# Performance work log

Hardware: AMD Instinct MI355X
Metric: run time of the kernel (lower is better)

## Reference

```python
import jax, jax.numpy as jnp
import numpy as np

N_NODES = 50000
N_EDGES = 800000
IN_DIM, HID_DIM, OUT_DIM = 128, 96, 96
NUM_GRAPHS = 64
NEG_SLOPE_ATT = 0.2   # GATConv internal leaky_relu
NEG_SLOPE_ACT = 0.01  # F.leaky_relu default between layers


def setup_inputs() -> dict:
    key = jax.random.key(0)
    ks = jax.random.split(key, 16)
    x = jax.random.normal(ks[0], (N_NODES, IN_DIM), dtype=jnp.float32)
    edge_index = jax.random.randint(ks[1], (2, N_EDGES), 0, N_NODES, dtype=jnp.int64)
    batch = jnp.sort(jax.random.randint(ks[2], (N_NODES,), 0, NUM_GRAPHS, dtype=jnp.int64))

    def glorot(k, shape):
        lim = np.sqrt(6.0 / (shape[0] + shape[-1]))
        return jax.random.uniform(k, shape, jnp.float32, -lim, lim)

    params = {}
    dims = [(IN_DIM, HID_DIM), (HID_DIM, HID_DIM), (HID_DIM, OUT_DIM)]
    for i, (di, do) in enumerate(dims, start=1):
        params[f"W{i}"] = glorot(ks[3 * i], (di, do))
        params[f"a_src{i}"] = glorot(ks[3 * i + 1], (do,))
        params[f"a_dst{i}"] = glorot(ks[3 * i + 2], (do,))
        params[f"b{i}"] = jnp.zeros((do,), jnp.float32)
    return {"x": x, "edge_index": edge_index, "batch": batch, **params}


def gat_conv(x, src, dst, W, a_src, a_dst, b):
    # x: [N, in], src/dst: [Etot] (self-loops included)
    h = x @ W                                   # [N, out]
    alpha_s = h @ a_src                         # [N]
    alpha_d = h @ a_dst                         # [N]
    e = jax.nn.leaky_relu(alpha_s[src] + alpha_d[dst], NEG_SLOPE_ATT)  # [Etot]
    # segment softmax over destination neighborhoods
    m = jax.ops.segment_max(e, dst, num_segments=N_NODES)
    ex = jnp.exp(e - m[dst])
    denom = jax.ops.segment_sum(ex, dst, num_segments=N_NODES)
    alpha = ex / (denom[dst] + 1e-16)           # [Etot]
    msg = alpha[:, None] * h[src]               # [Etot, out]
    out = jax.ops.segment_sum(msg, dst, num_segments=N_NODES)
    return out + b


def reference(x, edge_index, batch, W1, a_src1, a_dst1, b1, W2, a_src2, a_dst2, b2, W3, a_src3, a_dst3, b3):
    # add self loops once (PyG GATConv add_self_loops=True per layer; same edge set)
    sl = jnp.arange(N_NODES, dtype=edge_index.dtype)
    src = jnp.concatenate([edge_index[0], sl])
    dst = jnp.concatenate([edge_index[1], sl])

    h = jax.nn.leaky_relu(gat_conv(x, src, dst, W1, a_src1, a_dst1, b1), NEG_SLOPE_ACT)
    h = jax.nn.leaky_relu(gat_conv(h, src, dst, W2, a_src2, a_dst2, b2), NEG_SLOPE_ACT)
    h = gat_conv(h, src, dst, W3, a_src3, a_dst3, b3)

    # global mean pool over graphs
    sums = jax.ops.segment_sum(h, batch, num_segments=NUM_GRAPHS)       # [G, out]
    counts = jax.ops.segment_sum(jnp.ones((N_NODES,), h.dtype), batch, num_segments=NUM_GRAPHS)
    return sums / jnp.maximum(counts, 1.0)[:, None]
```

## Files before the change

### kernel.cpp

```cpp
#include <hip/hip_runtime.h>

#define N_NODES 50000
#define N_EDGES 800000
#define E_TOT   850000
#define IN0     128
#define HID     96
#define NUM_GRAPHS 64
#define NB      ((N_NODES + 1023) / 1024)

__device__ __forceinline__ float leaky(float x, float s) { return x > 0.f ? x : s * x; }

__global__ void count_deg(const int* __restrict__ dst, int* __restrict__ deg) {
    int e = blockIdx.x * blockDim.x + threadIdx.x;
    if (e >= E_TOT) return;
    int d = (e < N_EDGES) ? dst[e] : (e - N_EDGES);
    atomicAdd(&deg[d], 1);
}

__global__ __launch_bounds__(256) void block_sums(const int* __restrict__ deg, int* __restrict__ bsum) {
    int b = blockIdx.x, t = threadIdx.x;
    int base = b * 1024 + t * 4;
    int s = 0;
    if (base + 3 < N_NODES) {
        int4 v = *(const int4*)(deg + base);
        s = v.x + v.y + v.z + v.w;
    } else {
        for (int k = 0; k < 4; ++k) if (base + k < N_NODES) s += deg[base + k];
    }
#pragma unroll
    for (int w = 32; w >= 1; w >>= 1) s += __shfl_xor(s, w);
    __shared__ int ws[4];
    if ((t & 63) == 0) ws[t >> 6] = s;
    __syncthreads();
    if (t == 0) bsum[b] = ws[0] + ws[1] + ws[2] + ws[3];
}

__global__ void scan_partials(const int* __restrict__ bsum, int* __restrict__ excl, int* __restrict__ offs) {
    int t = threadIdx.x;
    int v = (t < NB) ? bsum[t] : 0;
    int incl = v;
#pragma unroll
    for (int d = 1; d < 64; d <<= 1) {
        int u = __shfl_up(incl, d);
        if (t >= d) incl += u;
    }
    if (t < NB) excl[t] = incl - v;
    if (t == 0) offs[N_NODES] = E_TOT;
}

__global__ __launch_bounds__(256) void write_offs(const int* __restrict__ deg,
                                                  const int* __restrict__ excl,
                                                  int* __restrict__ offs) {
    __shared__ int sh[256];
    int b = blockIdx.x, t = threadIdx.x;
    int base = b * 1024 + t * 4;
    int d0 = 0, d1 = 0, d2 = 0, d3 = 0;
    if (base + 3 < N_NODES) {
        int4 v = *(const int4*)(deg + base);
        d0 = v.x; d1 = v.y; d2 = v.z; d3 = v.w;
    } else {
        if (base     < N_NODES) d0 = deg[base];
        if (base + 1 < N_NODES) d1 = deg[base + 1];
        if (base + 2 < N_NODES) d2 = deg[base + 2];
    }
    int tsum = d0 + d1 + d2 + d3;
    sh[t] = tsum;
    __syncthreads();
    for (int off = 1; off < 256; off <<= 1) {
        int u = (t >= off) ? sh[t - off] : 0;
        __syncthreads();
        sh[t] += u;
        __syncthreads();
    }
    int ebase = excl[b] + sh[t] - tsum;
    if (base + 3 < N_NODES) {
        int4 o; o.x = ebase; o.y = ebase + d0; o.z = ebase + d0 + d1; o.w = ebase + d0 + d1 + d2;
        *(int4*)(offs + base) = o;
    } else {
        if (base     < N_NODES) offs[base]     = ebase;
        if (base + 1 < N_NODES) offs[base + 1] = ebase + d0;
        if (base + 2 < N_NODES) offs[base + 2] = ebase + d0 + d1;
    }
}

__global__ void scatter_edges(const int* __restrict__ src, const int* __restrict__ dst,
                              const int* __restrict__ offs, int* __restrict__ cursor,
                              int* __restrict__ csr) {
    int e = blockIdx.x * blockDim.x + threadIdx.x;
    if (e >= E_TOT) return;
    int s, d;
    if (e < N_EDGES) { s = src[e]; d = dst[e]; }
    else             { s = e - N_EDGES; d = s; }
    int pos = offs[d] + atomicAdd(&cursor[d], 1);
    csr[pos] = s;
}

template <int IN>
__global__ __launch_bounds__(512, 4) void gemm_tiled(
    const float* __restrict__ X, const float* __restrict__ W,
    const float* __restrict__ asrc, const float* __restrict__ adst,
    float* __restrict__ H, float* __restrict__ As, float* __restrict__ Ad) {
    __shared__ float Xs[64 * 36];
    __shared__ float Wt[96 * 36];
    int tid = threadIdx.x;
    int cx = tid & 31, ry = tid >> 5;
    int cbase = cx * 3;
    int rowBase = blockIdx.x * 64;
    const float* w0p = &Wt[(cbase + 0) * 36];
    const float* w1p = &Wt[(cbase + 1) * 36];
    const float* w2p = &Wt[(cbase + 2) * 36];
    const float* xsp = &Xs[ry * 4 * 36];
    float acc[4][3];
#pragma unroll
    for (int r = 0; r < 4; ++r)
#pragma unroll
        for (int j = 0; j < 3; ++j) acc[r][j] = 0.f;

    for (int t = 0; t < IN / 32; ++t) {
        int k0 = t * 32;
        __syncthreads();
        {
            int row = tid >> 3;
            int kk = (tid & 7) * 4;
            int grow = rowBase + row;
            float4 v = make_float4(0.f, 0.f, 0.f, 0.f);
            if (grow < N_NODES) v = *(const float4*)(X + (size_t)grow * IN + k0 + kk);
            *(float4*)(&Xs[row * 36 + kk]) = v;
        }
#pragma unroll
        for (int j = 0; j < 6; ++j) {
            int f = tid + j * 512;
            int kk = f / 96;
            int c = f - kk * 96;
            Wt[c * 36 + kk] = W[(size_t)(k0 + kk) * HID + c];
        }
        __syncthreads();
#pragma unroll 2
        for (int k = 0; k < 32; k += 4) {
            float4 w0 = *(const float4*)(w0p + k);
            float4 w1 = *(const float4*)(w1p + k);
            float4 w2 = *(const float4*)(w2p + k);
#pragma unroll
            for (int r = 0; r < 4; ++r) {
                float4 xv = *(const float4*)(xsp + r * 36 + k);
                acc[r][0] += xv.x * w0.x + xv.y * w0.y + xv.z * w0.z + xv.w * w0.w;
                acc[r][1] += xv.x * w1.x + xv.y * w1.y + xv.z * w1.z + xv.w * w1.w;
                acc[r][2] += xv.x * w2.x + xv.y * w2.y + xv.z * w2.z + xv.w * w2.w;
            }
        }
    }
    float a0 = asrc[cbase], a1 = asrc[cbase + 1], a2 = asrc[cbase + 2];
    float d0 = adst[cbase], d1 = adst[cbase + 1], d2 = adst[cbase + 2];
#pragma unroll
    for (int r = 0; r < 4; ++r) {
        int row = rowBase + ry * 4 + r;
        bool valid = row < N_NODES;
        float ps = acc[r][0] * a0 + acc[r][1] * a1 + acc[r][2] * a2;
        float pd = acc[r][0] * d0 + acc[r][1] * d1 + acc[r][2] * d2;
#pragma unroll
        for (int w = 16; w >= 1; w >>= 1) {
            ps += __shfl_xor(ps, w);
            pd += __shfl_xor(pd, w);
        }
        if (valid) {
            float* hr = H + (size_t)row * HID + cbase;
            hr[0] = acc[r][0]; hr[1] = acc[r][1]; hr[2] = acc[r][2];
            if (cx == 0) { As[row] = ps; Ad[row] = pd; }
        }
    }
}

__global__ __launch_bounds__(256) void aggregate(
    const float* __restrict__ H, const float* __restrict__ As, const float* __restrict__ Ad,
    const int* __restrict__ offs, const int* __restrict__ csr,
    const float* __restrict__ bias, float* __restrict__ Hout, int apply_leaky) {
    int team = (blockIdx.x * blockDim.x + threadIdx.x) >> 5;
    int lane = threadIdx.x & 31;
    int half = threadIdx.x & 32;
    int start = offs[team], end = offs[team + 1];
    float ad = Ad[team];
    float m = leaky(As[team] + ad, 0.2f);
    float acc0 = 0.f, acc1 = 0.f, acc2 = 0.f, denom = 0.f;
    int c = lane * 3;
    for (int base = start; base < end; base += 32) {
        int i = base + lane;
        bool valid = i < end;
        int s = valid ? csr[i] : 0;
        float ex = 0.f;
        if (valid) ex = __expf(leaky(As[s] + ad, 0.2f) - m);
        denom += ex;
        int cnt = min(32, end - base);
        int j = 0;
        for (; j + 8 <= cnt; j += 8) {
            float e[8]; int ss[8];
#pragma unroll
            for (int q = 0; q < 8; ++q) {
                e[q]  = __shfl(ex, half + j + q);
                ss[q] = __shfl(s,  half + j + q);
            }
            float v0[8], v1[8], v2[8];
#pragma unroll
            for (int q = 0; q < 8; ++q) {
                const float* p = H + (size_t)ss[q] * HID + c;
                v0[q] = p[0]; v1[q] = p[1]; v2[q] = p[2];
            }
#pragma unroll
            for (int q = 0; q < 8; ++q) {
                acc0 += e[q] * v0[q]; acc1 += e[q] * v1[q]; acc2 += e[q] * v2[q];
            }
        }
        for (; j + 4 <= cnt; j += 4) {
            float e[4]; int ss[4];
#pragma unroll
            for (int q = 0; q < 4; ++q) {
                e[q]  = __shfl(ex, half + j + q);
                ss[q] = __shfl(s,  half + j + q);
            }
            float v0[4], v1[4], v2[4];
#pragma unroll
            for (int q = 0; q < 4; ++q) {
                const float* p = H + (size_t)ss[q] * HID + c;
                v0[q] = p[0]; v1[q] = p[1]; v2[q] = p[2];
            }
#pragma unroll
            for (int q = 0; q < 4; ++q) {
                acc0 += e[q] * v0[q]; acc1 += e[q] * v1[q]; acc2 += e[q] * v2[q];
            }
        }
        for (; j < cnt; ++j) {
            float bex = __shfl(ex, half + j);
            int   bs  = __shfl(s,  half + j);
            const float* hp = H + (size_t)bs * HID + c;
            acc0 += bex * hp[0]; acc1 += bex * hp[1]; acc2 += bex * hp[2];
        }
    }
#pragma unroll
    for (int w = 16; w >= 1; w >>= 1) denom += __shfl_xor(denom, w);
    float inv = 1.f / (denom + 1e-16f);
    float o0 = acc0 * inv + bias[c];
    float o1 = acc1 * inv + bias[c + 1];
    float o2 = acc2 * inv + bias[c + 2];
    if (apply_leaky) { o0 = leaky(o0, 0.01f); o1 = leaky(o1, 0.01f); o2 = leaky(o2, 0.01f); }
    Hout[team * HID + c]     = o0;
    Hout[team * HID + c + 1] = o1;
    Hout[team * HID + c + 2] = o2;
}

__global__ __launch_bounds__(256) void pool_sum(
    const float* __restrict__ H, const int* __restrict__ batch,
    float* __restrict__ sums, float* __restrict__ counts) {
    int team = (blockIdx.x * blockDim.x + threadIdx.x) >> 5;
    int lane = threadIdx.x & 31;
    int c = lane * 3;
    int n0 = team * 32;
    if (n0 >= N_NODES) return;
    int n1 = min(n0 + 32, N_NODES);
    float a0 = 0.f, a1 = 0.f, a2 = 0.f;
    int cur = batch[n0], runlen = 0;
    for (int n = n0; n < n1; ++n) {
        int g = batch[n];
        if (g != cur) {
            atomicAdd(&sums[cur * HID + c],     a0);
            atomicAdd(&sums[cur * HID + c + 1], a1);
            atomicAdd(&sums[cur * HID + c + 2], a2);
            if (lane == 0) atomicAdd(&counts[cur], (float)runlen);
            a0 = a1 = a2 = 0.f; cur = g; runlen = 0;
        }
        const float* hp = H + (size_t)n * HID + c;
        a0 += hp[0]; a1 += hp[1]; a2 += hp[2];
        ++runlen;
    }
    atomicAdd(&sums[cur * HID + c],     a0);
    atomicAdd(&sums[cur * HID + c + 1], a1);
    atomicAdd(&sums[cur * HID + c + 2], a2);
    if (lane == 0) atomicAdd(&counts[cur], (float)runlen);
}

__global__ void finalize(const float* __restrict__ sums, const float* __restrict__ counts,
                         float* __restrict__ out) {
    int i = blockIdx.x * blockDim.x + threadIdx.x;
    if (i < NUM_GRAPHS * HID) out[i] = sums[i] / fmaxf(counts[i / HID], 1.f);
}

extern "C" void kernel_launch(void* const* d_in, const int* in_sizes, int n_in,
                              void* d_out, int out_size, void* d_ws, size_t ws_size,
                              hipStream_t stream) {
    const float* x     = (const float*)d_in[0];
    const int*   ei    = (const int*)d_in[1];
    const int*   srcI  = ei;
    const int*   dstI  = ei + N_EDGES;
    const int*   batch = (const int*)d_in[2];
    const float* W1 = (const float*)d_in[3],  *as1 = (const float*)d_in[4],
               * ad1 = (const float*)d_in[5], *b1  = (const float*)d_in[6];
    const float* W2 = (const float*)d_in[7],  *as2 = (const float*)d_in[8],
               * ad2 = (const float*)d_in[9], *b2  = (const float*)d_in[10];
    const float* W3 = (const float*)d_in[11], *as3 = (const float*)d_in[12],
               * ad3 = (const float*)d_in[13], *b3 = (const float*)d_in[14];
    float* out = (float*)d_out;

    char* p = (char*)d_ws;
    float* h0 = (float*)p;  p += (size_t)N_NODES * HID * 4;
    float* h1 = (float*)p;  p += (size_t)N_NODES * HID * 4;
    float* As = (float*)p;  p += (size_t)N_NODES * 4;
    float* Ad = (float*)p;  p += (size_t)N_NODES * 4;
    int* offs = (int*)p;    p += (size_t)(N_NODES + 4) * 4;
    int* csr  = (int*)p;    p += (size_t)E_TOT * 4;
    int* bsum = (int*)p;    p += 64 * 4;
    int* excl = (int*)p;    p += 64 * 4;
    char* zbase = p;
    float* sums   = (float*)p; p += (size_t)NUM_GRAPHS * HID * 4;
    float* counts = (float*)p; p += (size_t)NUM_GRAPHS * 4;
    int* deg    = (int*)p;  p += (size_t)N_NODES * 4;
    int* cursor = (int*)p;  p += (size_t)N_NODES * 4;
    size_t zbytes = (size_t)(p - zbase);

    hipMemsetAsync(zbase, 0, zbytes, stream);

    int eb = (E_TOT + 255) / 256;
    count_deg<<<eb, 256, 0, stream>>>(dstI, deg);
    block_sums<<<NB, 256, 0, stream>>>(deg, bsum);
    scan_partials<<<1, 64, 0, stream>>>(bsum, excl, offs);
    write_offs<<<NB, 256, 0, stream>>>(deg, excl, offs);
    scatter_edges<<<eb, 256, 0, stream>>>(srcI, dstI, offs, cursor, csr);

    int gemmGrid = (N_NODES + 63) / 64;
    int aggGrid  = (N_NODES * 32) / 256;

    gemm_tiled<IN0><<<gemmGrid, 512, 0, stream>>>(x, W1, as1, ad1, h0, As, Ad);
    aggregate<<<aggGrid, 256, 0, stream>>>(h0, As, Ad, offs, csr, b1, h1, 1);
    gemm_tiled<HID><<<gemmGrid, 512, 0, stream>>>(h1, W2, as2, ad2, h0, As, Ad);
    aggregate<<<aggGrid, 256, 0, stream>>>(h0, As, Ad, offs, csr, b2, h1, 1);
    gemm_tiled<HID><<<gemmGrid, 512, 0, stream>>>(h1, W3, as3, ad3, h0, As, Ad);
    aggregate<<<aggGrid, 256, 0, stream>>>(h0, As, Ad, offs, csr, b3, h1, 0);

    int teams = (N_NODES + 31) / 32;
    pool_sum<<<(teams * 32 + 255) / 256, 256, 0, stream>>>(h1, batch, sums, counts);
    finalize<<<(NUM_GRAPHS * HID + 255) / 256, 256, 0, stream>>>(sums, counts, out);
}
```

Measured before the change: 427.6 us.

## Keep full weight matrix resident in LDS and stream X rows from global

Restructures the dense transform so each block loads the entire transposed weight matrix into shared memory once, then each thread reads its four X rows directly from global memory with float4 loads. This removes the per-k-tile X staging and the two barriers per tile. In exchange, LDS use per block grows (up to about 50KB for IN=128), which may limit occupancy. X reads within a wavefront are now broadcast loads that rely on cache rather than coalesced shared staging.

```diff
diff --git a/kernel.cpp b/kernel.cpp
--- a/kernel.cpp
+++ b/kernel.cpp
@@ -96,64 +96,64 @@
 }
 
 template <int IN>
-__global__ __launch_bounds__(512, 4) void gemm_tiled(
+__global__ __launch_bounds__(512, 4) void gemm_wstat(
     const float* __restrict__ X, const float* __restrict__ W,
     const float* __restrict__ asrc, const float* __restrict__ adst,
     float* __restrict__ H, float* __restrict__ As, float* __restrict__ Ad) {
-    __shared__ float Xs[64 * 36];
-    __shared__ float Wt[96 * 36];
+    constexpr int S = IN + 4;
+    __shared__ float Wt[96 * S];
     int tid = threadIdx.x;
     int cx = tid & 31, ry = tid >> 5;
     int cbase = cx * 3;
     int rowBase = blockIdx.x * 64;
-    const float* w0p = &Wt[(cbase + 0) * 36];
-    const float* w1p = &Wt[(cbase + 1) * 36];
-    const float* w2p = &Wt[(cbase + 2) * 36];
-    const float* xsp = &Xs[ry * 4 * 36];
+#pragma unroll
+    for (int j = 0; j < (96 * IN) / 512; ++j) {
+        int f = j * 512 + tid;
+        int k = f / 96, c = f - k * 96;
+        Wt[c * S + k] = W[f];
+    }
+    __syncthreads();
+    const float* w0p = &Wt[(cbase + 0) * S];
+    const float* w1p = &Wt[(cbase + 1) * S];
+    const float* w2p = &Wt[(cbase + 2) * S];
+    int r0 = rowBase + ry * 4;
+    const float* x0 = X + (size_t)min(r0 + 0, N_NODES - 1) * IN;
+    const float* x1 = X + (size_t)min(r0 + 1, N_NODES - 1) * IN;
+    const float* x2 = X + (size_t)min(r0 + 2, N_NODES - 1) * IN;
+    const float* x3 = X + (size_t)min(r0 + 3, N_NODES - 1) * IN;
     float acc[4][3];
 #pragma unroll
     for (int r = 0; r < 4; ++r)
 #pragma unroll
         for (int j = 0; j < 3; ++j) acc[r][j] = 0.f;
 
-    for (int t = 0; t < IN / 32; ++t) {
-        int k0 = t * 32;
-        __syncthreads();
-        {
-            int row = tid >> 3;
-            int kk = (tid & 7) * 4;
-            int grow = rowBase + row;
-            float4 v = make_float4(0.f, 0.f, 0.f, 0.f);
-            if (grow < N_NODES) v = *(const float4*)(X + (size_t)grow * IN + k0 + kk);
-            *(float4*)(&Xs[row * 36 + kk]) = v;
-        }
-#pragma unroll
-        for (int j = 0; j < 6; ++j) {
-            int f = tid + j * 512;
-            int kk = f / 96;
-            int c = f - kk * 96;
-            Wt[c * 36 + kk] = W[(size_t)(k0 + kk) * HID + c];
-        }
-        __syncthreads();
 #pragma unroll 2
-        for (int k = 0; k < 32; k += 4) {
-            float4 w0 = *(const float4*)(w0p + k);
-            float4 w1 = *(const float4*)(w1p + k);
-            float4 w2 = *(const float4*)(w2p + k);
-#pragma unroll
-            for (int r = 0; r < 4; ++r) {
-                float4 xv = *(const float4*)(xsp + r * 36 + k);
-                acc[r][0] += xv.x * w0.x + xv.y * w0.y + xv.z * w0.z + xv.w * w0.w;
-                acc[r][1] += xv.x * w1.x + xv.y * w1.y + xv.z * w1.z + xv.w * w1.w;
-                acc[r][2] += xv.x * w2.x + xv.y * w2.y + xv.z * w2.z + xv.w * w2.w;
-            }
-        }
+    for (int k = 0; k < IN; k += 4) {
+        float4 w0 = *(const float4*)(w0p + k);
+        float4 w1 = *(const float4*)(w1p + k);
+        float4 w2 = *(const float4*)(w2p + k);
+        float4 xv0 = *(const float4*)(x0 + k);
+        float4 xv1 = *(const float4*)(x1 + k);
+        float4 xv2 = *(const float4*)(x2 + k);
+        float4 xv3 = *(const float4*)(x3 + k);
+        acc[0][0] += xv0.x * w0.x + xv0.y * w0.y + xv0.z * w0.z + xv0.w * w0.w;
+        acc[0][1] += xv0.x * w1.x + xv0.y * w1.y + xv0.z * w1.z + xv0.w * w1.w;
+        acc[0][2] += xv0.x * w2.x + xv0.y * w2.y + xv0.z * w2.z + xv0.w * w2.w;
+        acc[1][0] += xv1.x * w0.x + xv1.y * w0.y + xv1.z * w0.z + xv1.w * w0.w;
+        acc[1][1] += xv1.x * w1.x + xv1.y * w1.y + xv1.z * w1.z + xv1.w * w1.w;
+        acc[1][2] += xv1.x * w2.x + xv1.y * w2.y + xv1.z * w2.z + xv1.w * w2.w;
+        acc[2][0] += xv2.x * w0.x + xv2.y * w0.y + xv2.z * w0.z + xv2.w * w0.w;
+        acc[2][1] += xv2.x * w1.x + xv2.y * w1.y + xv2.z * w1.z + xv2.w * w1.w;
+        acc[2][2] += xv2.x * w2.x + xv2.y * w2.y + xv2.z * w2.z + xv2.w * w2.w;
+        acc[3][0] += xv3.x * w0.x + xv3.y * w0.y + xv3.z * w0.z + xv3.w * w0.w;
+        acc[3][1] += xv3.x * w1.x + xv3.y * w1.y + xv3.z * w1.z + xv3.w * w1.w;
+        acc[3][2] += xv3.x * w2.x + xv3.y * w2.y + xv3.z * w2.z + xv3.w * w2.w;
     }
     float a0 = asrc[cbase], a1 = asrc[cbase + 1], a2 = asrc[cbase + 2];
     float d0 = adst[cbase], d1 = adst[cbase + 1], d2 = adst[cbase + 2];
 #pragma unroll
     for (int r = 0; r < 4; ++r) {
-        int row = rowBase + ry * 4 + r;
+        int row = r0 + r;
         bool valid = row < N_NODES;
         float ps = acc[r][0] * a0 + acc[r][1] * a1 + acc[r][2] * a2;
         float pd = acc[r][0] * d0 + acc[r][1] * d1 + acc[r][2] * d2;
@@ -326,11 +326,11 @@
     int gemmGrid = (N_NODES + 63) / 64;
     int aggGrid  = (N_NODES * 32) / 256;
 
-    gemm_tiled<IN0><<<gemmGrid, 512, 0, stream>>>(x, W1, as1, ad1, h0, As, Ad);
+    gemm_wstat<IN0><<<gemmGrid, 512, 0, stream>>>(x, W1, as1, ad1, h0, As, Ad);
     aggregate<<<aggGrid, 256, 0, stream>>>(h0, As, Ad, offs, csr, b1, h1, 1);
-    gemm_tiled<HID><<<gemmGrid, 512, 0, stream>>>(h1, W2, as2, ad2, h0, As, Ad);
+    gemm_wstat<HID><<<gemmGrid, 512, 0, stream>>>(h1, W2, as2, ad2, h0, As, Ad);
     aggregate<<<aggGrid, 256, 0, stream>>>(h0, As, Ad, offs, csr, b2, h1, 1);
-    gemm_tiled<HID><<<gemmGrid, 512, 0, stream>>>(h1, W3, as3, ad3, h0, As, Ad);
+    gemm_wstat<HID><<<gemmGrid, 512, 0, stream>>>(h1, W3, as3, ad3, h0, As, Ad);
     aggregate<<<aggGrid, 256, 0, stream>>>(h0, As, Ad, offs, csr, b3, h1, 0);
 
     int teams = (N_NODES + 31) / 32;
```

After: 432.1 us. About the same (+1.1%).
